# Kernel tuning notes

Hardware: AMD Instinct MI355X
Metric: run time of the kernel (lower is better)

Reference implementation:

```python
import jax, jax.numpy as jnp
import numpy as np

HEADS = 4
DIM_HEAD = 32
EPS = 1e-5


def setup_inputs() -> dict:
    key = jax.random.key(0)
    ks = jax.random.split(key, 3)
    b, c, h, w = 32, 128, 128, 128
    hidden = HEADS * DIM_HEAD  # 128
    x = jax.random.normal(ks[0], (b, c, h, w), dtype=jnp.float32)
    Wqkv = jax.random.normal(ks[1], (3 * hidden, c), dtype=jnp.float32) * (1.0 / np.sqrt(c))
    Wout = jax.random.normal(ks[2], (c, hidden), dtype=jnp.float32) * (1.0 / np.sqrt(hidden))
    bout = jnp.zeros((c,), dtype=jnp.float32)
    g = jnp.ones((c,), dtype=jnp.float32)
    return {"x": x, "Wqkv": Wqkv, "Wout": Wout, "bout": bout, "g": g}


def reference(x, Wqkv, Wout, bout, g):
    b, c, h, w = x.shape
    n = h * w
    scale = DIM_HEAD ** -0.5
    # 1x1 conv (no bias) == channel GEMM
    qkv = jnp.einsum('oc,bchw->bohw', Wqkv, x)  # [b, 3*hidden, h, w]
    q, k, v = jnp.split(qkv, 3, axis=1)
    # b (h d) x y -> b h d n
    def to_heads(t):
        return t.reshape(b, HEADS, DIM_HEAD, n)
    q, k, v = to_heads(q), to_heads(k), to_heads(v)
    q = jax.nn.softmax(q, axis=-2) * scale   # softmax over per-head channel dim
    k = jax.nn.softmax(k, axis=-1)           # softmax over token dim
    v = v / n
    ctx = jnp.einsum('bhdn,bhen->bhde', k, v)   # [b, heads, d, e]
    out = jnp.einsum('bhde,bhdn->bhen', ctx, q)  # [b, heads, e, n]
    out = out.reshape(b, HEADS * DIM_HEAD, h, w)
    # output 1x1 conv with bias
    y = jnp.einsum('oc,bchw->bohw', Wout, out) + bout[None, :, None, None]
    # LayerNorm over channel dim (biased variance)
    mean = jnp.mean(y, axis=1, keepdims=True)
    var = jnp.var(y, axis=1, keepdims=True)
    return (y - mean) * jax.lax.rsqrt(var + EPS) * g[None, :, None, None]
```

## Files before the change

kernel.cpp:

```cpp
#include <hip/hip_runtime.h>
#include <math.h>


#define NCHUNK 64

typedef __attribute__((ext_vector_type(8))) short short8;
typedef __attribute__((ext_vector_type(4))) float f32x4;

__device__ __forceinline__ uint bf16r(float f) {
    uint u = __float_as_uint(f);
    return (u + 0x7FFFu + ((u >> 16) & 1u)) >> 16;
}
__device__ __forceinline__ float bf16f(uint h) { return __uint_as_float(h << 16); }
__device__ __forceinline__ uint2 bsplit(float f) {
    uint h = bf16r(f);
    float r = f - bf16f(h);
    return make_uint2(h, bf16r(r));
}
__device__ __forceinline__ uint2 bsplit_t(float f) {
    uint u = __float_as_uint(f);
    uint uh = u & 0xFFFF0000u;
    float r = f - __uint_as_float(uh);
    return make_uint2(uh >> 16, __float_as_uint(r) >> 16);
}
__device__ __forceinline__ uint bpack_t(float f) {
    uint u = __float_as_uint(f);
    uint uh = u & 0xFFFF0000u;
    float r = f - __uint_as_float(uh);
    return (uh >> 16) | (__float_as_uint(r) & 0xFFFF0000u);
}
__device__ __forceinline__ short8 lo8(uint4 a, uint4 b) {
    uint4 r;
    r.x = (a.x & 0xFFFFu) | (a.y << 16);
    r.y = (a.z & 0xFFFFu) | (a.w << 16);
    r.z = (b.x & 0xFFFFu) | (b.y << 16);
    r.w = (b.z & 0xFFFFu) | (b.w << 16);
    return __builtin_bit_cast(short8, r);
}
__device__ __forceinline__ short8 hi8(uint4 a, uint4 b) {
    uint4 r;
    r.x = (a.x >> 16) | (a.y & 0xFFFF0000u);
    r.y = (a.z >> 16) | (a.w & 0xFFFF0000u);
    r.z = (b.x >> 16) | (b.y & 0xFFFF0000u);
    r.w = (b.z >> 16) | (b.w & 0xFFFF0000u);
    return __builtin_bit_cast(short8, r);
}

__global__ __launch_bounds__(256)
void wsplit(const float* __restrict__ W, ushort* __restrict__ Wh,
            ushort* __restrict__ Wl, int n)
{
    const int base = (blockIdx.x * 256 + threadIdx.x) * 4;
    if (base + 3 < n) {
        const float4 f = *(const float4*)(W + base);
        const uint2 a = bsplit(f.x), b2 = bsplit(f.y), c = bsplit(f.z), d = bsplit(f.w);
        ushort4 hh; hh.x = (ushort)a.x; hh.y = (ushort)b2.x; hh.z = (ushort)c.x; hh.w = (ushort)d.x;
        ushort4 ll; ll.x = (ushort)a.y; ll.y = (ushort)b2.y; ll.z = (ushort)c.y; ll.w = (ushort)d.y;
        *(ushort4*)(Wh + base) = hh;
        *(ushort4*)(Wl + base) = ll;
    }
}

#define MFMA(A, B, C) __builtin_amdgcn_mfma_f32_16x16x32_bf16((A), (B), (C), 0, 0, 0)

__global__ __launch_bounds__(512, 1)
void la_k1(const float* __restrict__ x,
           const ushort* __restrict__ Wh, const ushort* __restrict__ Wl,
           float* __restrict__ Spart, float* __restrict__ Zpart)
{
    __shared__ __align__(16) char smb[163840];

    const int tid = threadIdx.x;
    const int b = blockIdx.y, chunk = blockIdx.x;
    const int w = tid >> 6, l = tid & 63;
    const int l15 = l & 15, lg = l >> 4;

    {
#pragma unroll
        for (int it = 0; it < 16; ++it) {
            const int q = tid + 512 * it;
            const int region = q >> 12;
            const int lin = (q & 4095) * 16;
            const int r = lin >> 8;
            const int dst = (region << 16) + (lin ^ ((r & 7) << 4));
            const ushort* src = (region ? Wl : Wh) + 128 * 128 + (lin >> 1);
            *(uint4*)(&smb[dst]) = *(const uint4*)src;
        }
    }

    f32x4 s2[2];
#pragma unroll
    for (int i = 0; i < 2; ++i) s2[i] = (f32x4){0.f, 0.f, 0.f, 0.f};
    float zrow[4];
#pragma unroll
    for (int i = 0; i < 4; ++i) zrow[i] = 0.f;

    const int hh = w >> 1, eh = w & 1;

    for (int t = 0; t < 8; ++t) {
        const int p0 = chunk * 256 + t * 32;
        {
            const float* xb = x + (size_t)b * 128 * 16384 + p0;
            const int cp = tid >> 3, j = tid & 7;
            const int pb = j * 4, c = cp * 2;
            const float4 a = *(const float4*)(xb + (size_t)c * 16384 + pb);
            const float4 bq = *(const float4*)(xb + (size_t)(c + 1) * 16384 + pb);
            const float av[4] = {a.x, a.y, a.z, a.w};
            const float bv[4] = {bq.x, bq.y, bq.z, bq.w};
#pragma unroll
            for (int pp = 0; pp < 4; ++pp) {
                const uint2 s0 = bsplit_t(av[pp]);
                const uint2 s1 = bsplit_t(bv[pp]);
                const int p = pb + pp;
                const int byt = (p * 256 + c * 2) ^ (((p ^ (p >> 3)) & 7) << 4);
                *(uint*)(&smb[131072 + byt])        = s0.x | (s1.x << 16);
                *(uint*)(&smb[131072 + 8192 + byt]) = s0.y | (s1.y << 16);
            }
        }
        __syncthreads();

        f32x4 acc[2][2];
#pragma unroll
        for (int rt = 0; rt < 2; ++rt)
#pragma unroll
            for (int ct = 0; ct < 2; ++ct) acc[rt][ct] = (f32x4){0.f, 0.f, 0.f, 0.f};
#pragma unroll
        for (int ks = 0; ks < 4; ++ks) {
            short8 Bh[2], Bl[2];
#pragma unroll
            for (int ct = 0; ct < 2; ++ct) {
                const int p = ct * 16 + l15;
                const int byt = (p * 256 + (ks * 32 + lg * 8) * 2) ^ (((p ^ (p >> 3)) & 7) << 4);
                Bh[ct] = *(const short8*)(&smb[131072 + byt]);
                Bl[ct] = *(const short8*)(&smb[131072 + 8192 + byt]);
            }
#pragma unroll
            for (int rt = 0; rt < 2; ++rt) {
                const int r = (w + rt * 8) * 16 + l15;
                const int abyt = (r * 256 + (ks * 32 + lg * 8) * 2) ^ ((r & 7) << 4);
                const short8 Ah_ = *(const short8*)(&smb[abyt]);
                const short8 Al_ = *(const short8*)(&smb[65536 + abyt]);
#pragma unroll
                for (int ct = 0; ct < 2; ++ct) {
                    acc[rt][ct] = MFMA(Ah_, Bh[ct], acc[rt][ct]);
                    acc[rt][ct] = MFMA(Ah_, Bl[ct], acc[rt][ct]);
                    acc[rt][ct] = MFMA(Al_, Bh[ct], acc[rt][ct]);
                }
            }
        }
        __syncthreads();

#pragma unroll
        for (int rt = 0; rt < 2; ++rt) {
            const bool isk = (rt == 0);
#pragma unroll
            for (int ct = 0; ct < 2; ++ct) {
                const int p = ct * 16 + l15;
#pragma unroll
                for (int i = 0; i < 4; ++i) {
                    float val = acc[rt][ct][i];
                    if (isk) {
                        val = expf(val);
                        zrow[i] += val;
                    }
                    const int r = w * 16 + lg * 4 + i;
                    const int byt = (r * 128 + p * 4) ^ ((r & 7) << 4);
                    *(uint*)(&smb[131072 + (isk ? 0 : 16384) + byt]) = bpack_t(val);
                }
            }
        }
        __syncthreads();

        {
            short8 A2h[2], A2l[2], B2h, B2l;
#pragma unroll
            for (int rt2 = 0; rt2 < 2; ++rt2) {
                const int r = hh * 32 + rt2 * 16 + l15;
                const int b0 = (r * 128 + lg * 32) ^ ((r & 7) << 4);
                const int b1 = (r * 128 + lg * 32 + 16) ^ ((r & 7) << 4);
                const uint4 q0 = *(const uint4*)(&smb[131072 + b0]);
                const uint4 q1 = *(const uint4*)(&smb[131072 + b1]);
                A2h[rt2] = lo8(q0, q1);
                A2l[rt2] = hi8(q0, q1);
            }
            {
                const int rv = hh * 32 + eh * 16 + l15;
                const int c0 = (rv * 128 + lg * 32) ^ ((rv & 7) << 4);
                const int c1 = (rv * 128 + lg * 32 + 16) ^ ((rv & 7) << 4);
                const uint4 r0 = *(const uint4*)(&smb[131072 + 16384 + c0]);
                const uint4 r1 = *(const uint4*)(&smb[131072 + 16384 + c1]);
                B2h = lo8(r0, r1);
                B2l = hi8(r0, r1);
            }
#pragma unroll
            for (int rt2 = 0; rt2 < 2; ++rt2) {
                s2[rt2] = MFMA(A2h[rt2], B2h, s2[rt2]);
                s2[rt2] = MFMA(A2h[rt2], B2l, s2[rt2]);
                s2[rt2] = MFMA(A2l[rt2], B2h, s2[rt2]);
            }
        }
        __syncthreads();
    }

    const size_t sbase = (((size_t)b * NCHUNK + chunk) * 4 + hh) * 1024;
#pragma unroll
    for (int rt2 = 0; rt2 < 2; ++rt2)
#pragma unroll
        for (int i = 0; i < 4; ++i) {
            const int d = rt2 * 16 + lg * 4 + i;
            const int e = eh * 16 + l15;
            Spart[sbase + d * 32 + e] = s2[rt2][i];
        }

#pragma unroll
    for (int i = 0; i < 4; ++i) {
        float z = zrow[i];
        z += __shfl_xor(z, 1, 64);
        z += __shfl_xor(z, 2, 64);
        z += __shfl_xor(z, 4, 64);
        z += __shfl_xor(z, 8, 64);
        if (l15 == 0)
            Zpart[((size_t)b * NCHUNK + chunk) * 128 + w * 16 + lg * 4 + i] = z;
    }
}

__global__ __launch_bounds__(256, 1)
void la_k1_reduce(const float* __restrict__ Spart, const float* __restrict__ Zpart,
                  float* __restrict__ ctxF)
{
    const int tid = threadIdx.x;
    const int b  = blockIdx.x >> 2;
    const int hh = blockIdx.x & 3;
    const int d  = tid >> 3;
    const int e0 = (tid & 7) << 2;
    float sx = 0.f, sy = 0.f, sz = 0.f, sw = 0.f, z = 0.f;
    for (int ch = 0; ch < NCHUNK; ++ch) {
        const size_t base = (((size_t)b * NCHUNK + ch) * 4 + hh) * 32 + d;
        const float4 v = *(const float4*)(Spart + base * 32 + e0);
        sx += v.x; sy += v.y; sz += v.z; sw += v.w;
        z += Zpart[base];
    }
    const float inv = 1.0f / (z * 16384.0f);
    float4 r; r.x = sx * inv; r.y = sy * inv; r.z = sz * inv; r.w = sw * inv;
    *(float4*)(ctxF + ((((size_t)b * 4 + hh) * 32 + d) << 5) + e0) = r;
}

__global__ __launch_bounds__(256, 1)
void la_mk(const float* __restrict__ Wout, const float* __restrict__ ctxF,
           ushort* __restrict__ Mh, ushort* __restrict__ Ml)
{
    __shared__ float ctxs[4096];
    const int b = blockIdx.x;
    const int tid = threadIdx.x;
#pragma unroll
    for (int i = 0; i < 4; ++i) {
        const int idx = (tid + 256 * i) * 4;
        *(float4*)(ctxs + idx) = *(const float4*)(ctxF + (size_t)b * 4096 + idx);
    }
    __syncthreads();
    const int cp = tid & 127;
    const int dh = tid >> 7;
#pragma unroll
    for (int hq = 0; hq < 2; ++hq) {
        const int h = dh * 2 + hq;
        float wrow[32];
#pragma unroll
        for (int e4 = 0; e4 < 8; ++e4) {
            const float4 wv = *(const float4*)(Wout + cp * 128 + h * 32 + e4 * 4);
            wrow[e4 * 4 + 0] = wv.x; wrow[e4 * 4 + 1] = wv.y;
            wrow[e4 * 4 + 2] = wv.z; wrow[e4 * 4 + 3] = wv.w;
        }
        for (int d = 0; d < 32; ++d) {
            float m = 0.f;
#pragma unroll
            for (int e = 0; e < 32; ++e)
                m += wrow[e] * ctxs[h * 1024 + d * 32 + e];
            const uint2 s = bsplit(m);
            const size_t mo = (size_t)b * 16384 + cp * 128 + h * 32 + d;
            Mh[mo] = (ushort)s.x;
            Ml[mo] = (ushort)s.y;
        }
    }
}

__device__ __forceinline__ int xswz64(int p, int cbyte) {
    return (p * 256 + cbyte) ^ (((p ^ (p >> 3)) & 7) << 4);
}
__device__ __forceinline__ int qswz(int p, int off) {
    return (p * 64 + off) ^ (((p >> 1) & 3) << 4);
}

__global__ __launch_bounds__(256, 4)
void la_k2(const float* __restrict__ x,
           const ushort* __restrict__ Wqh, const ushort* __restrict__ Wql,
           const ushort* __restrict__ Mh, const ushort* __restrict__ Ml,
           const float* __restrict__ bout, const float* __restrict__ g,
           float* __restrict__ outg)
{
    __shared__ __align__(16) char smb[32768];

    const int tid = threadIdx.x;
    const int b = blockIdx.y, chunk = blockIdx.x;
    const int p0 = chunk * 64;
    const int w = tid >> 6, l = tid & 63;
    const int l15 = l & 15, lg = l >> 4;
    const int ch2 = w >> 1;
    const int rp  = w & 1;

    short8 AqH[2][4], AqL[2][4];
#pragma unroll
    for (int t_ = 0; t_ < 2; ++t_)
#pragma unroll
        for (int ks = 0; ks < 4; ++ks) {
            const size_t aoff = (size_t)((2 * w + t_) * 16 + l15) * 128 + ks * 32 + lg * 8;
            AqH[t_][ks] = *(const short8*)(Wqh + aoff);
            AqL[t_][ks] = *(const short8*)(Wql + aoff);
        }

    {
        const float* xb = x + (size_t)b * 128 * 16384 + p0;
        const int j = tid & 15, gq = tid >> 4;
        const int pb = j * 4;
#pragma unroll
        for (int u = 0; u < 2; ++u) {
            const int cb = gq * 4 + u * 64;
            const float4 xv0 = *(const float4*)(xb + (size_t)(cb + 0) * 16384 + pb);
            const float4 xv1 = *(const float4*)(xb + (size_t)(cb + 1) * 16384 + pb);
            const float4 xv2 = *(const float4*)(xb + (size_t)(cb + 2) * 16384 + pb);
            const float4 xv3 = *(const float4*)(xb + (size_t)(cb + 3) * 16384 + pb);
            float rc[4][4];
            rc[0][0] = xv0.x; rc[0][1] = xv0.y; rc[0][2] = xv0.z; rc[0][3] = xv0.w;
            rc[1][0] = xv1.x; rc[1][1] = xv1.y; rc[1][2] = xv1.z; rc[1][3] = xv1.w;
            rc[2][0] = xv2.x; rc[2][1] = xv2.y; rc[2][2] = xv2.z; rc[2][3] = xv2.w;
            rc[3][0] = xv3.x; rc[3][1] = xv3.y; rc[3][2] = xv3.z; rc[3][3] = xv3.w;
#pragma unroll
            for (int pp = 0; pp < 4; ++pp) {
                const uint2 s0 = bsplit_t(rc[0][pp]);
                const uint2 s1 = bsplit_t(rc[1][pp]);
                const uint2 s2u = bsplit_t(rc[2][pp]);
                const uint2 s3 = bsplit_t(rc[3][pp]);
                const int p = pb + pp;
                const int byt = xswz64(p, cb * 2);
                *(uint2*)(&smb[byt])         = make_uint2(s0.x | (s1.x << 16), s2u.x | (s3.x << 16));
                *(uint2*)(&smb[16384 + byt]) = make_uint2(s0.y | (s1.y << 16), s2u.y | (s3.y << 16));
            }
        }
    }
    __syncthreads();

    f32x4 qacc[2][4];
#pragma unroll
    for (int t_ = 0; t_ < 2; ++t_)
#pragma unroll
        for (int ct = 0; ct < 4; ++ct) qacc[t_][ct] = (f32x4){0.f, 0.f, 0.f, 0.f};
#pragma unroll
    for (int ks = 0; ks < 4; ++ks) {
#pragma unroll
        for (int ct = 0; ct < 4; ++ct) {
            const int p = ct * 16 + l15;
            const int byt = xswz64(p, (ks * 32 + lg * 8) * 2);
            const short8 Bh_ = *(const short8*)(&smb[byt]);
            const short8 Bl_ = *(const short8*)(&smb[16384 + byt]);
#pragma unroll
            for (int t_ = 0; t_ < 2; ++t_) {
                qacc[t_][ct] = MFMA(AqH[t_][ks], Bh_, qacc[t_][ct]);
                qacc[t_][ct] = MFMA(AqH[t_][ks], Bl_, qacc[t_][ct]);
                qacc[t_][ct] = MFMA(AqL[t_][ks], Bh_, qacc[t_][ct]);
            }
        }
    }

    float vv[4][2][4];
#pragma unroll
    for (int ct = 0; ct < 4; ++ct) {
        float s = 0.f;
#pragma unroll
        for (int t_ = 0; t_ < 2; ++t_)
#pragma unroll
            for (int i = 0; i < 4; ++i) {
                vv[ct][t_][i] = expf(qacc[t_][ct][i]);
                s += vv[ct][t_][i];
            }
        s += __shfl_xor(s, 16, 64);
        s += __shfl_xor(s, 32, 64);
        const float inv = 0.17677669529663687f / s;
#pragma unroll
        for (int t_ = 0; t_ < 2; ++t_)
#pragma unroll
            for (int i = 0; i < 4; ++i) vv[ct][t_][i] *= inv;
    }
    __syncthreads();

#pragma unroll
    for (int ct = 0; ct < 4; ++ct) {
        const int p = ct * 16 + l15;
#pragma unroll
        for (int t_ = 0; t_ < 2; ++t_) {
            const uint2 a0 = bsplit_t(vv[ct][t_][0]);
            const uint2 a1 = bsplit_t(vv[ct][t_][1]);
            const uint2 a2 = bsplit_t(vv[ct][t_][2]);
            const uint2 a3 = bsplit_t(vv[ct][t_][3]);
            const int byt = w * 4096 + qswz(p, (t_ * 16 + lg * 4) * 2);
            *(uint2*)(&smb[byt])         = make_uint2(a0.x | (a1.x << 16), a2.x | (a3.x << 16));
            *(uint2*)(&smb[16384 + byt]) = make_uint2(a0.y | (a1.y << 16), a2.y | (a3.y << 16));
        }
    }
    __syncthreads();

    f32x4 yacc[4][2];
#pragma unroll
    for (int jj = 0; jj < 4; ++jj)
#pragma unroll
        for (int ct = 0; ct < 2; ++ct) yacc[jj][ct] = (f32x4){0.f, 0.f, 0.f, 0.f};
#pragma unroll
    for (int ks = 0; ks < 4; ++ks) {
        short8 Bh[2], Bl[2];
#pragma unroll
        for (int ct = 0; ct < 2; ++ct) {
            const int p = ch2 * 32 + ct * 16 + l15;
            const int byt = ks * 4096 + qswz(p, lg * 16);
            Bh[ct] = *(const short8*)(&smb[byt]);
            Bl[ct] = *(const short8*)(&smb[16384 + byt]);
        }
#pragma unroll
        for (int jj = 0; jj < 4; ++jj) {
            const int T = rp + 2 * jj;
            const size_t aoff = (size_t)b * 16384 + (size_t)(T * 16 + l15) * 128 + ks * 32 + lg * 8;
            const short8 Ah_ = *(const short8*)(Mh + aoff);
            const short8 Al_ = *(const short8*)(Ml + aoff);
#pragma unroll
            for (int ct = 0; ct < 2; ++ct) {
                yacc[jj][ct] = MFMA(Ah_, Bh[ct], yacc[jj][ct]);
                yacc[jj][ct] = MFMA(Ah_, Bl[ct], yacc[jj][ct]);
                yacc[jj][ct] = MFMA(Al_, Bh[ct], yacc[jj][ct]);
            }
        }
    }
    __syncthreads();

    float4 bo[4], gv[4];
#pragma unroll
    for (int jj = 0; jj < 4; ++jj) {
        const int rbase = (rp + 2 * jj) * 16 + lg * 4;
        bo[jj] = *(const float4*)(bout + rbase);
        gv[jj] = *(const float4*)(g + rbase);
    }
#pragma unroll
    for (int jj = 0; jj < 4; ++jj)
#pragma unroll
        for (int ct = 0; ct < 2; ++ct) {
            yacc[jj][ct][0] += bo[jj].x;
            yacc[jj][ct][1] += bo[jj].y;
            yacc[jj][ct][2] += bo[jj].z;
            yacc[jj][ct][3] += bo[jj].w;
        }
    float* lnred = (float*)smb;
    float sm[2], sq[2];
#pragma unroll
    for (int ct = 0; ct < 2; ++ct) {
        float s = 0.f, q = 0.f;
#pragma unroll
        for (int jj = 0; jj < 4; ++jj)
#pragma unroll
            for (int i = 0; i < 4; ++i) {
                const float yv = yacc[jj][ct][i];
                s += yv; q += yv * yv;
            }
        s += __shfl_xor(s, 16, 64); q += __shfl_xor(q, 16, 64);
        s += __shfl_xor(s, 32, 64); q += __shfl_xor(q, 32, 64);
        sm[ct] = s; sq[ct] = q;
    }
    if (lg == 0) {
#pragma unroll
        for (int ct = 0; ct < 2; ++ct) {
            const int p = ch2 * 32 + ct * 16 + l15;
            lnred[(p * 2 + rp) * 2 + 0] = sm[ct];
            lnred[(p * 2 + rp) * 2 + 1] = sq[ct];
        }
    }
    __syncthreads();
#pragma unroll
    for (int ct = 0; ct < 2; ++ct) {
        const int p = ch2 * 32 + ct * 16 + l15;
        const float st = lnred[(p * 2 + 0) * 2 + 0] + lnred[(p * 2 + 1) * 2 + 0];
        const float qt = lnred[(p * 2 + 0) * 2 + 1] + lnred[(p * 2 + 1) * 2 + 1];
        const float mean = st * (1.0f / 128.0f);
        const float var  = qt * (1.0f / 128.0f) - mean * mean;
        const float rstd = 1.0f / sqrtf(var + 1e-5f);
#pragma unroll
        for (int jj = 0; jj < 4; ++jj) {
            const int rbase = (rp + 2 * jj) * 16 + lg * 4;
            const float gg[4] = {gv[jj].x, gv[jj].y, gv[jj].z, gv[jj].w};
#pragma unroll
            for (int i = 0; i < 4; ++i) {
                const float val = (yacc[jj][ct][i] - mean) * rstd * gg[i];
                outg[((size_t)b * 128 + rbase + i) * 16384 + p0 + p] = val;
            }
        }
    }
}

extern "C" void kernel_launch(void* const* d_in, const int* in_sizes, int n_in,
                              void* d_out, int out_size, void* d_ws, size_t ws_size,
                              hipStream_t stream) {
    const float* x    = (const float*)d_in[0];
    const float* Wqkv = (const float*)d_in[1];
    const float* Wout = (const float*)d_in[2];
    const float* bout = (const float*)d_in[3];
    const float* g    = (const float*)d_in[4];
    float* out = (float*)d_out;

    float* Spart = (float*)d_ws;
    float* Zpart = Spart + (size_t)32 * NCHUNK * 4 * 32 * 32;
    float* ctxF  = Zpart + (size_t)32 * NCHUNK * 4 * 32;
    ushort* Wqh  = (ushort*)(ctxF + (size_t)32 * 4096);
    ushort* Wql  = Wqh + 384 * 128;
    ushort* Mh   = (ushort*)Spart;
    ushort* Ml   = Mh + (size_t)32 * 16384;
    (void)in_sizes; (void)n_in; (void)out_size; (void)ws_size;

    wsplit<<<dim3(48), 256, 0, stream>>>(Wqkv, Wqh, Wql, 384 * 128);
    la_k1<<<dim3(NCHUNK, 32), 512, 0, stream>>>(x, Wqh, Wql, Spart, Zpart);
    la_k1_reduce<<<dim3(128), 256, 0, stream>>>(Spart, Zpart, ctxF);
    la_mk<<<dim3(32), 256, 0, stream>>>(Wout, ctxF, Mh, Ml);
    la_k2<<<dim3(256, 32), 256, 0, stream>>>(x, Wqh, Wql, Mh, Ml, bout, g, out);
}
```

Before: 470.0 us.

## Make each wave own 16 tokens in la_k2 to drop block barriers

Restructures the second pass so each wave handles a private 16-token slice with its own LDS region. The wave computes all 128 q channels and all 128 output channels for that slice. This removes every __syncthreads and the cross-wave LayerNorm reduction through shared memory, since the channel reduction now stays within a wave via shuffles. In exchange, each wave reloads the full Wq and M fragments from global or L2 instead of keeping a register-resident share. Stores become 16-float rows per channel, which may reduce write coalescing.

```diff
diff --git a/kernel.cpp b/kernel.cpp
--- a/kernel.cpp
+++ b/kernel.cpp
@@ -283,219 +283,157 @@
     }
 }
 
-__device__ __forceinline__ int xswz64(int p, int cbyte) {
+__device__ __forceinline__ int wswz(int p, int cbyte) {
     return (p * 256 + cbyte) ^ (((p ^ (p >> 3)) & 7) << 4);
 }
-__device__ __forceinline__ int qswz(int p, int off) {
-    return (p * 64 + off) ^ (((p >> 1) & 3) << 4);
-}
 
 __global__ __launch_bounds__(256, 4)
-void la_k2(const float* __restrict__ x,
-           const ushort* __restrict__ Wqh, const ushort* __restrict__ Wql,
-           const ushort* __restrict__ Mh, const ushort* __restrict__ Ml,
-           const float* __restrict__ bout, const float* __restrict__ g,
-           float* __restrict__ outg)
+void la_k2w(const float* __restrict__ x,
+            const ushort* __restrict__ Wqh, const ushort* __restrict__ Wql,
+            const ushort* __restrict__ Mh, const ushort* __restrict__ Ml,
+            const float* __restrict__ bout, const float* __restrict__ g,
+            float* __restrict__ outg)
 {
     __shared__ __align__(16) char smb[32768];
 
     const int tid = threadIdx.x;
     const int b = blockIdx.y, chunk = blockIdx.x;
-    const int p0 = chunk * 64;
     const int w = tid >> 6, l = tid & 63;
     const int l15 = l & 15, lg = l >> 4;
-    const int ch2 = w >> 1;
-    const int rp  = w & 1;
-
-    short8 AqH[2][4], AqL[2][4];
-#pragma unroll
-    for (int t_ = 0; t_ < 2; ++t_)
-#pragma unroll
-        for (int ks = 0; ks < 4; ++ks) {
-            const size_t aoff = (size_t)((2 * w + t_) * 16 + l15) * 128 + ks * 32 + lg * 8;
-            AqH[t_][ks] = *(const short8*)(Wqh + aoff);
-            AqL[t_][ks] = *(const short8*)(Wql + aoff);
-        }
+    const int p0 = chunk * 64 + w * 16;
+    char* wlds = smb + w * 8192;
 
     {
         const float* xb = x + (size_t)b * 128 * 16384 + p0;
-        const int j = tid & 15, gq = tid >> 4;
-        const int pb = j * 4;
-#pragma unroll
-        for (int u = 0; u < 2; ++u) {
-            const int cb = gq * 4 + u * 64;
-            const float4 xv0 = *(const float4*)(xb + (size_t)(cb + 0) * 16384 + pb);
-            const float4 xv1 = *(const float4*)(xb + (size_t)(cb + 1) * 16384 + pb);
-            const float4 xv2 = *(const float4*)(xb + (size_t)(cb + 2) * 16384 + pb);
-            const float4 xv3 = *(const float4*)(xb + (size_t)(cb + 3) * 16384 + pb);
-            float rc[4][4];
-            rc[0][0] = xv0.x; rc[0][1] = xv0.y; rc[0][2] = xv0.z; rc[0][3] = xv0.w;
-            rc[1][0] = xv1.x; rc[1][1] = xv1.y; rc[1][2] = xv1.z; rc[1][3] = xv1.w;
-            rc[2][0] = xv2.x; rc[2][1] = xv2.y; rc[2][2] = xv2.z; rc[2][3] = xv2.w;
-            rc[3][0] = xv3.x; rc[3][1] = xv3.y; rc[3][2] = xv3.z; rc[3][3] = xv3.w;
-#pragma unroll
-            for (int pp = 0; pp < 4; ++pp) {
-                const uint2 s0 = bsplit_t(rc[0][pp]);
-                const uint2 s1 = bsplit_t(rc[1][pp]);
-                const uint2 s2u = bsplit_t(rc[2][pp]);
-                const uint2 s3 = bsplit_t(rc[3][pp]);
-                const int p = pb + pp;
-                const int byt = xswz64(p, cb * 2);
-                *(uint2*)(&smb[byt])         = make_uint2(s0.x | (s1.x << 16), s2u.x | (s3.x << 16));
-                *(uint2*)(&smb[16384 + byt]) = make_uint2(s0.y | (s1.y << 16), s2u.y | (s3.y << 16));
-            }
-        }
-    }
-    __syncthreads();
-
-    f32x4 qacc[2][4];
-#pragma unroll
-    for (int t_ = 0; t_ < 2; ++t_)
-#pragma unroll
-        for (int ct = 0; ct < 4; ++ct) qacc[t_][ct] = (f32x4){0.f, 0.f, 0.f, 0.f};
+        const int p4 = l & 3;
+        const int rg = l >> 2;
+        float4 xv[8];
+#pragma unroll
+        for (int rr = 0; rr < 8; ++rr)
+            xv[rr] = *(const float4*)(xb + (size_t)(rg * 8 + rr) * 16384 + p4 * 4);
+        float rcv[8][4];
+#pragma unroll
+        for (int rr = 0; rr < 8; ++rr) {
+            rcv[rr][0] = xv[rr].x; rcv[rr][1] = xv[rr].y;
+            rcv[rr][2] = xv[rr].z; rcv[rr][3] = xv[rr].w;
+        }
+#pragma unroll
+        for (int pp = 0; pp < 4; ++pp) {
+            const int p = p4 * 4 + pp;
+#pragma unroll
+            for (int q = 0; q < 2; ++q) {
+                const uint2 s0 = bsplit_t(rcv[q * 4 + 0][pp]);
+                const uint2 s1 = bsplit_t(rcv[q * 4 + 1][pp]);
+                const uint2 s2u = bsplit_t(rcv[q * 4 + 2][pp]);
+                const uint2 s3 = bsplit_t(rcv[q * 4 + 3][pp]);
+                const int byt = wswz(p, (rg * 8 + q * 4) * 2);
+                *(uint2*)(&wlds[byt])        = make_uint2(s0.x | (s1.x << 16), s2u.x | (s3.x << 16));
+                *(uint2*)(&wlds[4096 + byt]) = make_uint2(s0.y | (s1.y << 16), s2u.y | (s3.y << 16));
+            }
+        }
+    }
+
+    f32x4 qacc[8];
+#pragma unroll
+    for (int T = 0; T < 8; ++T) qacc[T] = (f32x4){0.f, 0.f, 0.f, 0.f};
 #pragma unroll
     for (int ks = 0; ks < 4; ++ks) {
-#pragma unroll
-        for (int ct = 0; ct < 4; ++ct) {
-            const int p = ct * 16 + l15;
-            const int byt = xswz64(p, (ks * 32 + lg * 8) * 2);
-            const short8 Bh_ = *(const short8*)(&smb[byt]);
-            const short8 Bl_ = *(const short8*)(&smb[16384 + byt]);
-#pragma unroll
-            for (int t_ = 0; t_ < 2; ++t_) {
-                qacc[t_][ct] = MFMA(AqH[t_][ks], Bh_, qacc[t_][ct]);
-                qacc[t_][ct] = MFMA(AqH[t_][ks], Bl_, qacc[t_][ct]);
-                qacc[t_][ct] = MFMA(AqL[t_][ks], Bh_, qacc[t_][ct]);
-            }
-        }
-    }
-
-    float vv[4][2][4];
-#pragma unroll
-    for (int ct = 0; ct < 4; ++ct) {
+        const int byt = wswz(l15, (ks * 32 + lg * 8) * 2);
+        const short8 Bh_ = *(const short8*)(&wlds[byt]);
+        const short8 Bl_ = *(const short8*)(&wlds[4096 + byt]);
+#pragma unroll
+        for (int T = 0; T < 8; ++T) {
+            const size_t aoff = (size_t)(T * 16 + l15) * 128 + ks * 32 + lg * 8;
+            const short8 Ah_ = *(const short8*)(Wqh + aoff);
+            const short8 Al_ = *(const short8*)(Wql + aoff);
+            qacc[T] = MFMA(Ah_, Bh_, qacc[T]);
+            qacc[T] = MFMA(Ah_, Bl_, qacc[T]);
+            qacc[T] = MFMA(Al_, Bh_, qacc[T]);
+        }
+    }
+
+    float vv[8][4];
+#pragma unroll
+    for (int T = 0; T < 8; ++T)
+#pragma unroll
+        for (int i = 0; i < 4; ++i) vv[T][i] = expf(qacc[T][i]);
+#pragma unroll
+    for (int h = 0; h < 4; ++h) {
         float s = 0.f;
 #pragma unroll
-        for (int t_ = 0; t_ < 2; ++t_)
-#pragma unroll
-            for (int i = 0; i < 4; ++i) {
-                vv[ct][t_][i] = expf(qacc[t_][ct][i]);
-                s += vv[ct][t_][i];
-            }
+        for (int tt = 0; tt < 2; ++tt)
+#pragma unroll
+            for (int i = 0; i < 4; ++i) s += vv[h * 2 + tt][i];
         s += __shfl_xor(s, 16, 64);
         s += __shfl_xor(s, 32, 64);
         const float inv = 0.17677669529663687f / s;
 #pragma unroll
-        for (int t_ = 0; t_ < 2; ++t_)
-#pragma unroll
-            for (int i = 0; i < 4; ++i) vv[ct][t_][i] *= inv;
-    }
-    __syncthreads();
-
-#pragma unroll
-    for (int ct = 0; ct < 4; ++ct) {
-        const int p = ct * 16 + l15;
-#pragma unroll
-        for (int t_ = 0; t_ < 2; ++t_) {
-            const uint2 a0 = bsplit_t(vv[ct][t_][0]);
-            const uint2 a1 = bsplit_t(vv[ct][t_][1]);
-            const uint2 a2 = bsplit_t(vv[ct][t_][2]);
-            const uint2 a3 = bsplit_t(vv[ct][t_][3]);
-            const int byt = w * 4096 + qswz(p, (t_ * 16 + lg * 4) * 2);
-            *(uint2*)(&smb[byt])         = make_uint2(a0.x | (a1.x << 16), a2.x | (a3.x << 16));
-            *(uint2*)(&smb[16384 + byt]) = make_uint2(a0.y | (a1.y << 16), a2.y | (a3.y << 16));
-        }
-    }
-    __syncthreads();
-
-    f32x4 yacc[4][2];
-#pragma unroll
-    for (int jj = 0; jj < 4; ++jj)
-#pragma unroll
-        for (int ct = 0; ct < 2; ++ct) yacc[jj][ct] = (f32x4){0.f, 0.f, 0.f, 0.f};
+        for (int tt = 0; tt < 2; ++tt)
+#pragma unroll
+            for (int i = 0; i < 4; ++i) vv[h * 2 + tt][i] *= inv;
+    }
+
+#pragma unroll
+    for (int T = 0; T < 8; ++T) {
+        const uint2 a0 = bsplit_t(vv[T][0]);
+        const uint2 a1 = bsplit_t(vv[T][1]);
+        const uint2 a2 = bsplit_t(vv[T][2]);
+        const uint2 a3 = bsplit_t(vv[T][3]);
+        const int byt = wswz(l15, (T * 16 + lg * 4) * 2);
+        *(uint2*)(&wlds[byt])        = make_uint2(a0.x | (a1.x << 16), a2.x | (a3.x << 16));
+        *(uint2*)(&wlds[4096 + byt]) = make_uint2(a0.y | (a1.y << 16), a2.y | (a3.y << 16));
+    }
+
+    f32x4 yacc[8];
+#pragma unroll
+    for (int T = 0; T < 8; ++T) yacc[T] = (f32x4){0.f, 0.f, 0.f, 0.f};
 #pragma unroll
     for (int ks = 0; ks < 4; ++ks) {
-        short8 Bh[2], Bl[2];
-#pragma unroll
-        for (int ct = 0; ct < 2; ++ct) {
-            const int p = ch2 * 32 + ct * 16 + l15;
-            const int byt = ks * 4096 + qswz(p, lg * 16);
-            Bh[ct] = *(const short8*)(&smb[byt]);
-            Bl[ct] = *(const short8*)(&smb[16384 + byt]);
-        }
-#pragma unroll
-        for (int jj = 0; jj < 4; ++jj) {
-            const int T = rp + 2 * jj;
+        const int byt = wswz(l15, (ks * 32 + lg * 8) * 2);
+        const short8 Bh_ = *(const short8*)(&wlds[byt]);
+        const short8 Bl_ = *(const short8*)(&wlds[4096 + byt]);
+#pragma unroll
+        for (int T = 0; T < 8; ++T) {
             const size_t aoff = (size_t)b * 16384 + (size_t)(T * 16 + l15) * 128 + ks * 32 + lg * 8;
             const short8 Ah_ = *(const short8*)(Mh + aoff);
             const short8 Al_ = *(const short8*)(Ml + aoff);
-#pragma unroll
-            for (int ct = 0; ct < 2; ++ct) {
-                yacc[jj][ct] = MFMA(Ah_, Bh[ct], yacc[jj][ct]);
-                yacc[jj][ct] = MFMA(Ah_, Bl[ct], yacc[jj][ct]);
-                yacc[jj][ct] = MFMA(Al_, Bh[ct], yacc[jj][ct]);
-            }
-        }
-    }
-    __syncthreads();
-
-    float4 bo[4], gv[4];
-#pragma unroll
-    for (int jj = 0; jj < 4; ++jj) {
-        const int rbase = (rp + 2 * jj) * 16 + lg * 4;
-        bo[jj] = *(const float4*)(bout + rbase);
-        gv[jj] = *(const float4*)(g + rbase);
-    }
-#pragma unroll
-    for (int jj = 0; jj < 4; ++jj)
-#pragma unroll
-        for (int ct = 0; ct < 2; ++ct) {
-            yacc[jj][ct][0] += bo[jj].x;
-            yacc[jj][ct][1] += bo[jj].y;
-            yacc[jj][ct][2] += bo[jj].z;
-            yacc[jj][ct][3] += bo[jj].w;
-        }
-    float* lnred = (float*)smb;
-    float sm[2], sq[2];
-#pragma unroll
-    for (int ct = 0; ct < 2; ++ct) {
-        float s = 0.f, q = 0.f;
-#pragma unroll
-        for (int jj = 0; jj < 4; ++jj)
-#pragma unroll
-            for (int i = 0; i < 4; ++i) {
-                const float yv = yacc[jj][ct][i];
-                s += yv; q += yv * yv;
-            }
-        s += __shfl_xor(s, 16, 64); q += __shfl_xor(q, 16, 64);
-        s += __shfl_xor(s, 32, 64); q += __shfl_xor(q, 32, 64);
-        sm[ct] = s; sq[ct] = q;
-    }
-    if (lg == 0) {
-#pragma unroll
-        for (int ct = 0; ct < 2; ++ct) {
-            const int p = ch2 * 32 + ct * 16 + l15;
-            lnred[(p * 2 + rp) * 2 + 0] = sm[ct];
-            lnred[(p * 2 + rp) * 2 + 1] = sq[ct];
-        }
-    }
-    __syncthreads();
-#pragma unroll
-    for (int ct = 0; ct < 2; ++ct) {
-        const int p = ch2 * 32 + ct * 16 + l15;
-        const float st = lnred[(p * 2 + 0) * 2 + 0] + lnred[(p * 2 + 1) * 2 + 0];
-        const float qt = lnred[(p * 2 + 0) * 2 + 1] + lnred[(p * 2 + 1) * 2 + 1];
-        const float mean = st * (1.0f / 128.0f);
-        const float var  = qt * (1.0f / 128.0f) - mean * mean;
-        const float rstd = 1.0f / sqrtf(var + 1e-5f);
-#pragma unroll
-        for (int jj = 0; jj < 4; ++jj) {
-            const int rbase = (rp + 2 * jj) * 16 + lg * 4;
-            const float gg[4] = {gv[jj].x, gv[jj].y, gv[jj].z, gv[jj].w};
-#pragma unroll
-            for (int i = 0; i < 4; ++i) {
-                const float val = (yacc[jj][ct][i] - mean) * rstd * gg[i];
-                outg[((size_t)b * 128 + rbase + i) * 16384 + p0 + p] = val;
-            }
+            yacc[T] = MFMA(Ah_, Bh_, yacc[T]);
+            yacc[T] = MFMA(Ah_, Bl_, yacc[T]);
+            yacc[T] = MFMA(Al_, Bh_, yacc[T]);
+        }
+    }
+
+    float4 bo[8], gv[8];
+#pragma unroll
+    for (int T = 0; T < 8; ++T) {
+        bo[T] = *(const float4*)(bout + T * 16 + lg * 4);
+        gv[T] = *(const float4*)(g + T * 16 + lg * 4);
+    }
+    float s = 0.f, q = 0.f;
+#pragma unroll
+    for (int T = 0; T < 8; ++T) {
+        yacc[T][0] += bo[T].x; yacc[T][1] += bo[T].y;
+        yacc[T][2] += bo[T].z; yacc[T][3] += bo[T].w;
+#pragma unroll
+        for (int i = 0; i < 4; ++i) {
+            const float yv = yacc[T][i];
+            s += yv; q += yv * yv;
+        }
+    }
+    s += __shfl_xor(s, 16, 64); q += __shfl_xor(q, 16, 64);
+    s += __shfl_xor(s, 32, 64); q += __shfl_xor(q, 32, 64);
+    const float mean = s * (1.0f / 128.0f);
+    const float var  = q * (1.0f / 128.0f) - mean * mean;
+    const float rstd = 1.0f / sqrtf(var + 1e-5f);
+
+#pragma unroll
+    for (int T = 0; T < 8; ++T) {
+        const float gg[4] = {gv[T].x, gv[T].y, gv[T].z, gv[T].w};
+#pragma unroll
+        for (int i = 0; i < 4; ++i) {
+            const int o = T * 16 + lg * 4 + i;
+            outg[((size_t)b * 128 + o) * 16384 + p0 + l15] =
+                (yacc[T][i] - mean) * rstd * gg[i];
         }
     }
 }
@@ -523,5 +461,5 @@
     la_k1<<<dim3(NCHUNK, 32), 512, 0, stream>>>(x, Wqh, Wql, Spart, Zpart);
     la_k1_reduce<<<dim3(128), 256, 0, stream>>>(Spart, Zpart, ctxF);
     la_mk<<<dim3(32), 256, 0, stream>>>(Wout, ctxF, Mh, Ml);
-    la_k2<<<dim3(256, 32), 256, 0, stream>>>(x, Wqh, Wql, Mh, Ml, bout, g, out);
-}
+    la_k2w<<<dim3(256, 32), 256, 0, stream>>>(x, Wqh, Wql, Mh, Ml, bout, g, out);
+}
```

After: 755.4 us. 1.61x slower.

## Process two token tiles per la_k2 block and use packed bf16 split conversion

Applied to the files above, without the earlier changes.

la_k2 now loops over two 64-token tiles per block and launches half as many blocks, so the per-block load of the Wq hi/lo weight fragments into registers is spread over twice the work. The manual truncating bf16 hi/lo split is replaced by a paired round-to-nearest conversion through __float22bfloat162_rn, which can map to packed convert instructions. The tile loop adds an extra barrier per iteration and halves the number of blocks, which may reduce latency hiding. The split now rounds the high part instead of truncating, which changes numerics slightly.

```diff
diff --git a/kernel.cpp b/kernel.cpp
--- a/kernel.cpp
+++ b/kernel.cpp
@@ -1,4 +1,5 @@
 #include <hip/hip_runtime.h>
+#include <hip/hip_bf16.h>
 #include <math.h>
 
 
@@ -17,17 +18,23 @@
     float r = f - bf16f(h);
     return make_uint2(h, bf16r(r));
 }
-__device__ __forceinline__ uint2 bsplit_t(float f) {
-    uint u = __float_as_uint(f);
-    uint uh = u & 0xFFFF0000u;
-    float r = f - __uint_as_float(uh);
-    return make_uint2(uh >> 16, __float_as_uint(r) >> 16);
-}
 __device__ __forceinline__ uint bpack_t(float f) {
     uint u = __float_as_uint(f);
     uint uh = u & 0xFFFF0000u;
     float r = f - __uint_as_float(uh);
     return (uh >> 16) | (__float_as_uint(r) & 0xFFFF0000u);
+}
+__device__ __forceinline__ uint b2u(__hip_bfloat162 v) {
+    uint r; __builtin_memcpy(&r, &v, 4); return r;
+}
+__device__ __forceinline__ uint pkpair(float a, float b, uint* lp) {
+    float2 f2; f2.x = a; f2.y = b;
+    const uint hp = b2u(__float22bfloat162_rn(f2));
+    float2 r2;
+    r2.x = a - __uint_as_float(hp << 16);
+    r2.y = b - __uint_as_float(hp & 0xFFFF0000u);
+    *lp = b2u(__float22bfloat162_rn(r2));
+    return hp;
 }
 __device__ __forceinline__ short8 lo8(uint4 a, uint4 b) {
     uint4 r;
@@ -109,12 +116,12 @@
             const float bv[4] = {bq.x, bq.y, bq.z, bq.w};
 #pragma unroll
             for (int pp = 0; pp < 4; ++pp) {
-                const uint2 s0 = bsplit_t(av[pp]);
-                const uint2 s1 = bsplit_t(bv[pp]);
+                uint lp;
+                const uint hp = pkpair(av[pp], bv[pp], &lp);
                 const int p = pb + pp;
                 const int byt = (p * 256 + c * 2) ^ (((p ^ (p >> 3)) & 7) << 4);
-                *(uint*)(&smb[131072 + byt])        = s0.x | (s1.x << 16);
-                *(uint*)(&smb[131072 + 8192 + byt]) = s0.y | (s1.y << 16);
+                *(uint*)(&smb[131072 + byt])        = hp;
+                *(uint*)(&smb[131072 + 8192 + byt]) = lp;
             }
         }
         __syncthreads();
@@ -301,7 +308,6 @@
 
     const int tid = threadIdx.x;
     const int b = blockIdx.y, chunk = blockIdx.x;
-    const int p0 = chunk * 64;
     const int w = tid >> 6, l = tid & 63;
     const int l15 = l & 15, lg = l >> 4;
     const int ch2 = w >> 1;
@@ -317,186 +323,189 @@
             AqL[t_][ks] = *(const short8*)(Wql + aoff);
         }
 
-    {
-        const float* xb = x + (size_t)b * 128 * 16384 + p0;
-        const int j = tid & 15, gq = tid >> 4;
-        const int pb = j * 4;
-#pragma unroll
-        for (int u = 0; u < 2; ++u) {
-            const int cb = gq * 4 + u * 64;
-            const float4 xv0 = *(const float4*)(xb + (size_t)(cb + 0) * 16384 + pb);
-            const float4 xv1 = *(const float4*)(xb + (size_t)(cb + 1) * 16384 + pb);
-            const float4 xv2 = *(const float4*)(xb + (size_t)(cb + 2) * 16384 + pb);
-            const float4 xv3 = *(const float4*)(xb + (size_t)(cb + 3) * 16384 + pb);
-            float rc[4][4];
-            rc[0][0] = xv0.x; rc[0][1] = xv0.y; rc[0][2] = xv0.z; rc[0][3] = xv0.w;
-            rc[1][0] = xv1.x; rc[1][1] = xv1.y; rc[1][2] = xv1.z; rc[1][3] = xv1.w;
-            rc[2][0] = xv2.x; rc[2][1] = xv2.y; rc[2][2] = xv2.z; rc[2][3] = xv2.w;
-            rc[3][0] = xv3.x; rc[3][1] = xv3.y; rc[3][2] = xv3.z; rc[3][3] = xv3.w;
-#pragma unroll
-            for (int pp = 0; pp < 4; ++pp) {
-                const uint2 s0 = bsplit_t(rc[0][pp]);
-                const uint2 s1 = bsplit_t(rc[1][pp]);
-                const uint2 s2u = bsplit_t(rc[2][pp]);
-                const uint2 s3 = bsplit_t(rc[3][pp]);
-                const int p = pb + pp;
-                const int byt = xswz64(p, cb * 2);
-                *(uint2*)(&smb[byt])         = make_uint2(s0.x | (s1.x << 16), s2u.x | (s3.x << 16));
-                *(uint2*)(&smb[16384 + byt]) = make_uint2(s0.y | (s1.y << 16), s2u.y | (s3.y << 16));
-            }
-        }
-    }
-    __syncthreads();
-
-    f32x4 qacc[2][4];
-#pragma unroll
-    for (int t_ = 0; t_ < 2; ++t_)
-#pragma unroll
-        for (int ct = 0; ct < 4; ++ct) qacc[t_][ct] = (f32x4){0.f, 0.f, 0.f, 0.f};
-#pragma unroll
-    for (int ks = 0; ks < 4; ++ks) {
+    for (int it = 0; it < 2; ++it) {
+        const int p0 = chunk * 128 + it * 64;
+
+        {
+            const float* xb = x + (size_t)b * 128 * 16384 + p0;
+            const int j = tid & 15, gq = tid >> 4;
+            const int pb = j * 4;
+#pragma unroll
+            for (int u = 0; u < 2; ++u) {
+                const int cb = gq * 4 + u * 64;
+                const float4 xv0 = *(const float4*)(xb + (size_t)(cb + 0) * 16384 + pb);
+                const float4 xv1 = *(const float4*)(xb + (size_t)(cb + 1) * 16384 + pb);
+                const float4 xv2 = *(const float4*)(xb + (size_t)(cb + 2) * 16384 + pb);
+                const float4 xv3 = *(const float4*)(xb + (size_t)(cb + 3) * 16384 + pb);
+                float rc[4][4];
+                rc[0][0] = xv0.x; rc[0][1] = xv0.y; rc[0][2] = xv0.z; rc[0][3] = xv0.w;
+                rc[1][0] = xv1.x; rc[1][1] = xv1.y; rc[1][2] = xv1.z; rc[1][3] = xv1.w;
+                rc[2][0] = xv2.x; rc[2][1] = xv2.y; rc[2][2] = xv2.z; rc[2][3] = xv2.w;
+                rc[3][0] = xv3.x; rc[3][1] = xv3.y; rc[3][2] = xv3.z; rc[3][3] = xv3.w;
+#pragma unroll
+                for (int pp = 0; pp < 4; ++pp) {
+                    uint l01, l23;
+                    const uint h01 = pkpair(rc[0][pp], rc[1][pp], &l01);
+                    const uint h23 = pkpair(rc[2][pp], rc[3][pp], &l23);
+                    const int p = pb + pp;
+                    const int byt = xswz64(p, cb * 2);
+                    *(uint2*)(&smb[byt])         = make_uint2(h01, h23);
+                    *(uint2*)(&smb[16384 + byt]) = make_uint2(l01, l23);
+                }
+            }
+        }
+        __syncthreads();
+
+        f32x4 qacc[2][4];
+#pragma unroll
+        for (int t_ = 0; t_ < 2; ++t_)
+#pragma unroll
+            for (int ct = 0; ct < 4; ++ct) qacc[t_][ct] = (f32x4){0.f, 0.f, 0.f, 0.f};
+#pragma unroll
+        for (int ks = 0; ks < 4; ++ks) {
+#pragma unroll
+            for (int ct = 0; ct < 4; ++ct) {
+                const int p = ct * 16 + l15;
+                const int byt = xswz64(p, (ks * 32 + lg * 8) * 2);
+                const short8 Bh_ = *(const short8*)(&smb[byt]);
+                const short8 Bl_ = *(const short8*)(&smb[16384 + byt]);
+#pragma unroll
+                for (int t_ = 0; t_ < 2; ++t_) {
+                    qacc[t_][ct] = MFMA(AqH[t_][ks], Bh_, qacc[t_][ct]);
+                    qacc[t_][ct] = MFMA(AqH[t_][ks], Bl_, qacc[t_][ct]);
+                    qacc[t_][ct] = MFMA(AqL[t_][ks], Bh_, qacc[t_][ct]);
+                }
+            }
+        }
+
+        float vv[4][2][4];
+#pragma unroll
+        for (int ct = 0; ct < 4; ++ct) {
+            float s = 0.f;
+#pragma unroll
+            for (int t_ = 0; t_ < 2; ++t_)
+#pragma unroll
+                for (int i = 0; i < 4; ++i) {
+                    vv[ct][t_][i] = expf(qacc[t_][ct][i]);
+                    s += vv[ct][t_][i];
+                }
+            s += __shfl_xor(s, 16, 64);
+            s += __shfl_xor(s, 32, 64);
+            const float inv = 0.17677669529663687f / s;
+#pragma unroll
+            for (int t_ = 0; t_ < 2; ++t_)
+#pragma unroll
+                for (int i = 0; i < 4; ++i) vv[ct][t_][i] *= inv;
+        }
+        __syncthreads();
+
 #pragma unroll
         for (int ct = 0; ct < 4; ++ct) {
             const int p = ct * 16 + l15;
-            const int byt = xswz64(p, (ks * 32 + lg * 8) * 2);
-            const short8 Bh_ = *(const short8*)(&smb[byt]);
-            const short8 Bl_ = *(const short8*)(&smb[16384 + byt]);
 #pragma unroll
             for (int t_ = 0; t_ < 2; ++t_) {
-                qacc[t_][ct] = MFMA(AqH[t_][ks], Bh_, qacc[t_][ct]);
-                qacc[t_][ct] = MFMA(AqH[t_][ks], Bl_, qacc[t_][ct]);
-                qacc[t_][ct] = MFMA(AqL[t_][ks], Bh_, qacc[t_][ct]);
-            }
-        }
-    }
-
-    float vv[4][2][4];
-#pragma unroll
-    for (int ct = 0; ct < 4; ++ct) {
-        float s = 0.f;
-#pragma unroll
-        for (int t_ = 0; t_ < 2; ++t_)
-#pragma unroll
-            for (int i = 0; i < 4; ++i) {
-                vv[ct][t_][i] = expf(qacc[t_][ct][i]);
-                s += vv[ct][t_][i];
-            }
-        s += __shfl_xor(s, 16, 64);
-        s += __shfl_xor(s, 32, 64);
-        const float inv = 0.17677669529663687f / s;
-#pragma unroll
-        for (int t_ = 0; t_ < 2; ++t_)
-#pragma unroll
-            for (int i = 0; i < 4; ++i) vv[ct][t_][i] *= inv;
-    }
-    __syncthreads();
-
-#pragma unroll
-    for (int ct = 0; ct < 4; ++ct) {
-        const int p = ct * 16 + l15;
-#pragma unroll
-        for (int t_ = 0; t_ < 2; ++t_) {
-            const uint2 a0 = bsplit_t(vv[ct][t_][0]);
-            const uint2 a1 = bsplit_t(vv[ct][t_][1]);
-            const uint2 a2 = bsplit_t(vv[ct][t_][2]);
-            const uint2 a3 = bsplit_t(vv[ct][t_][3]);
-            const int byt = w * 4096 + qswz(p, (t_ * 16 + lg * 4) * 2);
-            *(uint2*)(&smb[byt])         = make_uint2(a0.x | (a1.x << 16), a2.x | (a3.x << 16));
-            *(uint2*)(&smb[16384 + byt]) = make_uint2(a0.y | (a1.y << 16), a2.y | (a3.y << 16));
-        }
-    }
-    __syncthreads();
-
-    f32x4 yacc[4][2];
-#pragma unroll
-    for (int jj = 0; jj < 4; ++jj)
-#pragma unroll
-        for (int ct = 0; ct < 2; ++ct) yacc[jj][ct] = (f32x4){0.f, 0.f, 0.f, 0.f};
-#pragma unroll
-    for (int ks = 0; ks < 4; ++ks) {
-        short8 Bh[2], Bl[2];
+                uint l01, l23;
+                const uint h01 = pkpair(vv[ct][t_][0], vv[ct][t_][1], &l01);
+                const uint h23 = pkpair(vv[ct][t_][2], vv[ct][t_][3], &l23);
+                const int byt = w * 4096 + qswz(p, (t_ * 16 + lg * 4) * 2);
+                *(uint2*)(&smb[byt])         = make_uint2(h01, h23);
+                *(uint2*)(&smb[16384 + byt]) = make_uint2(l01, l23);
+            }
+        }
+        __syncthreads();
+
+        f32x4 yacc[4][2];
+#pragma unroll
+        for (int jj = 0; jj < 4; ++jj)
+#pragma unroll
+            for (int ct = 0; ct < 2; ++ct) yacc[jj][ct] = (f32x4){0.f, 0.f, 0.f, 0.f};
+#pragma unroll
+        for (int ks = 0; ks < 4; ++ks) {
+            short8 Bh[2], Bl[2];
+#pragma unroll
+            for (int ct = 0; ct < 2; ++ct) {
+                const int p = ch2 * 32 + ct * 16 + l15;
+                const int byt = ks * 4096 + qswz(p, lg * 16);
+                Bh[ct] = *(const short8*)(&smb[byt]);
+                Bl[ct] = *(const short8*)(&smb[16384 + byt]);
+            }
+#pragma unroll
+            for (int jj = 0; jj < 4; ++jj) {
+                const int T = rp + 2 * jj;
+                const size_t aoff = (size_t)b * 16384 + (size_t)(T * 16 + l15) * 128 + ks * 32 + lg * 8;
+                const short8 Ah_ = *(const short8*)(Mh + aoff);
+                const short8 Al_ = *(const short8*)(Ml + aoff);
+#pragma unroll
+                for (int ct = 0; ct < 2; ++ct) {
+                    yacc[jj][ct] = MFMA(Ah_, Bh[ct], yacc[jj][ct]);
+                    yacc[jj][ct] = MFMA(Ah_, Bl[ct], yacc[jj][ct]);
+                    yacc[jj][ct] = MFMA(Al_, Bh[ct], yacc[jj][ct]);
+                }
+            }
+        }
+        __syncthreads();
+
+        float4 bo[4], gv[4];
+#pragma unroll
+        for (int jj = 0; jj < 4; ++jj) {
+            const int rbase = (rp + 2 * jj) * 16 + lg * 4;
+            bo[jj] = *(const float4*)(bout + rbase);
+            gv[jj] = *(const float4*)(g + rbase);
+        }
+#pragma unroll
+        for (int jj = 0; jj < 4; ++jj)
+#pragma unroll
+            for (int ct = 0; ct < 2; ++ct) {
+                yacc[jj][ct][0] += bo[jj].x;
+                yacc[jj][ct][1] += bo[jj].y;
+                yacc[jj][ct][2] += bo[jj].z;
+                yacc[jj][ct][3] += bo[jj].w;
+            }
+        float* lnred = (float*)smb;
+        float sm[2], sq[2];
+#pragma unroll
+        for (int ct = 0; ct < 2; ++ct) {
+            float s = 0.f, q = 0.f;
+#pragma unroll
+            for (int jj = 0; jj < 4; ++jj)
+#pragma unroll
+                for (int i = 0; i < 4; ++i) {
+                    const float yv = yacc[jj][ct][i];
+                    s += yv; q += yv * yv;
+                }
+            s += __shfl_xor(s, 16, 64); q += __shfl_xor(q, 16, 64);
+            s += __shfl_xor(s, 32, 64); q += __shfl_xor(q, 32, 64);
+            sm[ct] = s; sq[ct] = q;
+        }
+        if (lg == 0) {
+#pragma unroll
+            for (int ct = 0; ct < 2; ++ct) {
+                const int p = ch2 * 32 + ct * 16 + l15;
+                lnred[(p * 2 + rp) * 2 + 0] = sm[ct];
+                lnred[(p * 2 + rp) * 2 + 1] = sq[ct];
+            }
+        }
+        __syncthreads();
 #pragma unroll
         for (int ct = 0; ct < 2; ++ct) {
             const int p = ch2 * 32 + ct * 16 + l15;
-            const int byt = ks * 4096 + qswz(p, lg * 16);
-            Bh[ct] = *(const short8*)(&smb[byt]);
-            Bl[ct] = *(const short8*)(&smb[16384 + byt]);
-        }
-#pragma unroll
-        for (int jj = 0; jj < 4; ++jj) {
-            const int T = rp + 2 * jj;
-            const size_t aoff = (size_t)b * 16384 + (size_t)(T * 16 + l15) * 128 + ks * 32 + lg * 8;
-            const short8 Ah_ = *(const short8*)(Mh + aoff);
-            const short8 Al_ = *(const short8*)(Ml + aoff);
-#pragma unroll
-            for (int ct = 0; ct < 2; ++ct) {
-                yacc[jj][ct] = MFMA(Ah_, Bh[ct], yacc[jj][ct]);
-                yacc[jj][ct] = MFMA(Ah_, Bl[ct], yacc[jj][ct]);
-                yacc[jj][ct] = MFMA(Al_, Bh[ct], yacc[jj][ct]);
-            }
-        }
-    }
-    __syncthreads();
-
-    float4 bo[4], gv[4];
-#pragma unroll
-    for (int jj = 0; jj < 4; ++jj) {
-        const int rbase = (rp + 2 * jj) * 16 + lg * 4;
-        bo[jj] = *(const float4*)(bout + rbase);
-        gv[jj] = *(const float4*)(g + rbase);
-    }
-#pragma unroll
-    for (int jj = 0; jj < 4; ++jj)
-#pragma unroll
-        for (int ct = 0; ct < 2; ++ct) {
-            yacc[jj][ct][0] += bo[jj].x;
-            yacc[jj][ct][1] += bo[jj].y;
-            yacc[jj][ct][2] += bo[jj].z;
-            yacc[jj][ct][3] += bo[jj].w;
-        }
-    float* lnred = (float*)smb;
-    float sm[2], sq[2];
-#pragma unroll
-    for (int ct = 0; ct < 2; ++ct) {
-        float s = 0.f, q = 0.f;
-#pragma unroll
-        for (int jj = 0; jj < 4; ++jj)
-#pragma unroll
-            for (int i = 0; i < 4; ++i) {
-                const float yv = yacc[jj][ct][i];
-                s += yv; q += yv * yv;
-            }
-        s += __shfl_xor(s, 16, 64); q += __shfl_xor(q, 16, 64);
-        s += __shfl_xor(s, 32, 64); q += __shfl_xor(q, 32, 64);
-        sm[ct] = s; sq[ct] = q;
-    }
-    if (lg == 0) {
-#pragma unroll
-        for (int ct = 0; ct < 2; ++ct) {
-            const int p = ch2 * 32 + ct * 16 + l15;
-            lnred[(p * 2 + rp) * 2 + 0] = sm[ct];
-            lnred[(p * 2 + rp) * 2 + 1] = sq[ct];
-        }
-    }
-    __syncthreads();
-#pragma unroll
-    for (int ct = 0; ct < 2; ++ct) {
-        const int p = ch2 * 32 + ct * 16 + l15;
-        const float st = lnred[(p * 2 + 0) * 2 + 0] + lnred[(p * 2 + 1) * 2 + 0];
-        const float qt = lnred[(p * 2 + 0) * 2 + 1] + lnred[(p * 2 + 1) * 2 + 1];
-        const float mean = st * (1.0f / 128.0f);
-        const float var  = qt * (1.0f / 128.0f) - mean * mean;
-        const float rstd = 1.0f / sqrtf(var + 1e-5f);
-#pragma unroll
-        for (int jj = 0; jj < 4; ++jj) {
-            const int rbase = (rp + 2 * jj) * 16 + lg * 4;
-            const float gg[4] = {gv[jj].x, gv[jj].y, gv[jj].z, gv[jj].w};
-#pragma unroll
-            for (int i = 0; i < 4; ++i) {
-                const float val = (yacc[jj][ct][i] - mean) * rstd * gg[i];
-                outg[((size_t)b * 128 + rbase + i) * 16384 + p0 + p] = val;
-            }
-        }
+            const float st = lnred[(p * 2 + 0) * 2 + 0] + lnred[(p * 2 + 1) * 2 + 0];
+            const float qt = lnred[(p * 2 + 0) * 2 + 1] + lnred[(p * 2 + 1) * 2 + 1];
+            const float mean = st * (1.0f / 128.0f);
+            const float var  = qt * (1.0f / 128.0f) - mean * mean;
+            const float rstd = 1.0f / sqrtf(var + 1e-5f);
+#pragma unroll
+            for (int jj = 0; jj < 4; ++jj) {
+                const int rbase = (rp + 2 * jj) * 16 + lg * 4;
+                const float gg[4] = {gv[jj].x, gv[jj].y, gv[jj].z, gv[jj].w};
+#pragma unroll
+                for (int i = 0; i < 4; ++i) {
+                    const float val = (yacc[jj][ct][i] - mean) * rstd * gg[i];
+                    outg[((size_t)b * 128 + rbase + i) * 16384 + p0 + p] = val;
+                }
+            }
+        }
+        __syncthreads();
     }
 }
 
@@ -523,5 +532,5 @@
     la_k1<<<dim3(NCHUNK, 32), 512, 0, stream>>>(x, Wqh, Wql, Spart, Zpart);
     la_k1_reduce<<<dim3(128), 256, 0, stream>>>(Spart, Zpart, ctxF);
     la_mk<<<dim3(32), 256, 0, stream>>>(Wout, ctxF, Mh, Ml);
-    la_k2<<<dim3(256, 32), 256, 0, stream>>>(x, Wqh, Wql, Mh, Ml, bout, g, out);
-}
+    la_k2<<<dim3(128, 32), 256, 0, stream>>>(x, Wqh, Wql, Mh, Ml, bout, g, out);
+}
```

After: 1.130 ms. 2.4x slower.
